# Optimization experiments

Hardware: AMD Instinct MI355X
Metric: run time of the kernel (lower is better)

## Reference

```python
import jax, jax.numpy as jnp
import numpy as np
from jax import lax

B, IN_CH, OUT_CH, H, W = 32, 128, 256, 64, 64
STYLE_CH, TDIM, G = 512, 512, 32
GN_EPS, MOD_EPS = 1e-5, 1e-8
DN = ('NCHW', 'OIHW', 'NCHW')


def swish(x):
    return x * jax.nn.sigmoid(x)


def group_norm(x, gamma, beta):
    n, c, h, w = x.shape
    xr = x.reshape(n, G, c // G, h, w)
    mu = xr.mean(axis=(2, 3, 4), keepdims=True)
    var = xr.var(axis=(2, 3, 4), keepdims=True)
    xn = ((xr - mu) * lax.rsqrt(var + GN_EPS)).reshape(n, c, h, w)
    return xn * gamma[None, :, None, None] + beta[None, :, None, None]


def conv3x3(x, w, b):
    y = lax.conv_general_dilated(x, w, (1, 1), ((1, 1), (1, 1)), dimension_numbers=DN)
    return y + b[None, :, None, None]


def setup_inputs() -> dict:
    key = jax.random.key(0)
    ks = jax.random.split(key, 16)
    s = 0.05
    return {
        'x': jax.random.normal(ks[0], (B, IN_CH, H, W), jnp.float32),
        'temb': jax.random.normal(ks[1], (B, TDIM), jnp.float32),
        'style': jax.random.normal(ks[2], (B, STYLE_CH), jnp.float32),
        'gn1_g': jnp.ones((IN_CH,), jnp.float32),
        'gn1_b': jnp.zeros((IN_CH,), jnp.float32),
        'conv1_w': jax.random.normal(ks[3], (OUT_CH, IN_CH, 3, 3), jnp.float32) * s,
        'conv1_b': jnp.zeros((OUT_CH,), jnp.float32),
        'temb_w': jax.random.normal(ks[4], (OUT_CH, TDIM), jnp.float32) * s,
        'temb_b': jnp.zeros((OUT_CH,), jnp.float32),
        'gn2_g': jnp.ones((OUT_CH,), jnp.float32),
        'gn2_b': jnp.zeros((OUT_CH,), jnp.float32),
        'style_w': jax.random.normal(ks[5], (OUT_CH, STYLE_CH), jnp.float32) * s,
        'style_b': jnp.zeros((OUT_CH,), jnp.float32),
        'mod_w': jax.random.normal(ks[6], (OUT_CH, OUT_CH, 3, 3), jnp.float32) * s,
        'sc_w': jax.random.normal(ks[7], (OUT_CH, IN_CH, 1, 1), jnp.float32) * s,
        'sc_b': jnp.zeros((OUT_CH,), jnp.float32),
    }


def reference(x, temb, style, gn1_g, gn1_b, conv1_w, conv1_b, temb_w, temb_b,
              gn2_g, gn2_b, style_w, style_b, mod_w, sc_w, sc_b):
    # block1: GN -> Swish -> Conv3x3
    h = conv3x3(swish(group_norm(x, gn1_g, gn1_b)), conv1_w, conv1_b)
    # temb projection: Swish -> Linear, broadcast over HxW
    h = h + (swish(temb) @ temb_w.T + temb_b)[:, :, None, None]
    # block2: GN -> Swish -> Dropout(0) [identity]
    h = swish(group_norm(h, gn2_g, gn2_b))
    # modulated + demodulated per-sample conv (StyleGAN2-style)
    style2 = style @ style_w.T + style_b                       # (b, out_ch)
    wmod = mod_w[None] * (style2[:, None, :, None, None] + 1.0)  # (b, o, i, kh, kw)
    d = lax.rsqrt((wmod ** 2).sum(axis=(2, 3, 4), keepdims=True) + MOD_EPS)
    wmod = wmod * d
    conv1s = lambda xi, wi: lax.conv_general_dilated(
        xi[None], wi, (1, 1), ((1, 1), (1, 1)), dimension_numbers=DN)[0]
    h = jax.vmap(conv1s)(h, wmod)                              # per-sample conv
    # shortcut 1x1 conv (in_ch != out_ch)
    sc = lax.conv_general_dilated(x, sc_w, (1, 1), ((0, 0), (0, 0)), dimension_numbers=DN)
    sc = sc + sc_b[None, :, None, None]
    return h + sc
```

## Files before the change

### kernel.cpp

```cpp
#include <hip/hip_runtime.h>
#include <cstdint>

typedef unsigned short u16;
typedef unsigned int   u32;

typedef __attribute__((ext_vector_type(8))) short bf16x8;
typedef __attribute__((ext_vector_type(4))) float f32x4;

#define DEV __device__ __forceinline__

static constexpr int HP = 66, WP = 66;

DEV u16 f2bf(float f) {
  u32 u = __float_as_uint(f);
  u32 r = (u + 0x7fffu + ((u >> 16) & 1u)) >> 16;
  return (u16)r;
}
DEV float bf2f(u16 v) { return __uint_as_float((u32)v << 16); }

DEV void gload_lds16(const void* g, void* s) {
  __builtin_amdgcn_global_load_lds(
      (const __attribute__((address_space(1))) void*)g,
      (__attribute__((address_space(3))) void*)s, 16, 0, 0);
}

__global__ __launch_bounds__(256) void repack_w_kernel(const float* __restrict__ src,
                                                       u16* __restrict__ dst,
                                                       int Cin, int K, int total,
                                                       int ksq, int kdim) {
  for (int idx = blockIdx.x * 256 + threadIdx.x; idx < total; idx += gridDim.x * 256) {
    int co = idx / K;
    int r  = idx - co * K;
    int s  = r / Cin;
    int ci = r - s * Cin;
    int ky = s / kdim, kx = s - ky * kdim;
    dst[idx] = f2bf(src[(co * Cin + ci) * ksq + ky * kdim + kx]);
  }
}

__global__ __launch_bounds__(256) void modw_ss_kernel(const float* __restrict__ w,
                                                      float* __restrict__ SS_T) {
  int o = blockIdx.x, i = threadIdx.x;
  const float* p = w + (size_t)(o * 256 + i) * 9;
  float s = 0.f;
#pragma unroll
  for (int k = 0; k < 9; ++k) s += p[k] * p[k];
  SS_T[i * 256 + o] = s;
}

__global__ __launch_bounds__(256) void style_mvec_kernel(const float* __restrict__ style,
                                                         const float* __restrict__ style_w,
                                                         const float* __restrict__ style_b,
                                                         float* __restrict__ mvec) {
  __shared__ float st[512];
  int b = blockIdx.x, t = threadIdx.x;
  for (int k = t; k < 512; k += 256) st[k] = style[b * 512 + k];
  __syncthreads();
  const float4* wr = (const float4*)(style_w + t * 512);
  float acc = 0.f;
  for (int k = 0; k < 128; ++k) {
    float4 w4 = wr[k];
    acc += w4.x * st[k*4] + w4.y * st[k*4+1] + w4.z * st[k*4+2] + w4.w * st[k*4+3];
  }
  mvec[b * 256 + t] = acc + style_b[t] + 1.f;
}

__global__ __launch_bounds__(256) void demod_kernel(const float* __restrict__ mvec,
                                                    const float* __restrict__ SS_T,
                                                    float* __restrict__ dvec) {
  __shared__ float m2[256];
  int b = blockIdx.x, t = threadIdx.x;
  float mv = mvec[b * 256 + t];
  m2[t] = mv * mv;
  __syncthreads();
  float acc = 0.f;
  for (int i = 0; i < 256; ++i) acc += m2[i] * SS_T[i * 256 + t];
  dvec[b * 256 + t] = rsqrtf(acc + 1e-8f);
}

__global__ __launch_bounds__(256) void scale_sc_kernel(const float* __restrict__ sc_w,
                                                       const float* __restrict__ dvec,
                                                       u16* __restrict__ scTb) {
  int idx = blockIdx.x * 256 + threadIdx.x;
  int ci = idx & 127;
  int co = (idx >> 7) & 255;
  int b  = idx >> 15;
  scTb[idx] = f2bf(sc_w[co * 128 + ci] / dvec[b * 256 + co]);
}

__global__ __launch_bounds__(256) void temb_proj_kernel(const float* __restrict__ temb,
                                                        const float* __restrict__ temb_w,
                                                        const float* __restrict__ temb_b,
                                                        const float* __restrict__ conv1_b,
                                                        float* __restrict__ tb2) {
  __shared__ float sw[512];
  int b = blockIdx.x, t = threadIdx.x;
  for (int k = t; k < 512; k += 256) {
    float v = temb[b * 512 + k];
    sw[k] = v / (1.f + __expf(-v));
  }
  __syncthreads();
  const float4* wr = (const float4*)(temb_w + t * 512);
  float acc = 0.f;
  for (int k = 0; k < 128; ++k) {
    float4 w4 = wr[k];
    acc += w4.x * sw[k*4] + w4.y * sw[k*4+1] + w4.z * sw[k*4+2] + w4.w * sw[k*4+3];
  }
  tb2[b * 256 + t] = acc + temb_b[t] + conv1_b[t];
}

template <int C>
__global__ __launch_bounds__(256) void halo_zero_kernel(u16* __restrict__ buf) {
  int idx = blockIdx.x * 256 + threadIdx.x;
  const int GR = C / 8;
  if (idx >= 32 * 260 * GR) return;
  int g = idx % GR;
  int p = (idx / GR) % 260;
  int b = idx / (GR * 260);
  int y, x;
  if (p < 66)       { y = 0;        x = p; }
  else if (p < 132) { y = 65;       x = p - 66; }
  else if (p < 196) { y = p - 131;  x = 0; }
  else              { y = p - 195;  x = 65; }
  uint4 z; z.x = 0; z.y = 0; z.z = 0; z.w = 0;
  *(uint4*)(buf + (((size_t)b * HP + y) * WP + x) * C + g * 8) = z;
}

__global__ __launch_bounds__(256) void gn1_stats_kernel(const float* __restrict__ x,
                                                        float2* __restrict__ st1) {
  int bg = blockIdx.x;
  const float4* p = (const float4*)(x + (size_t)bg * 16384);
  float s = 0.f, s2 = 0.f;
  for (int i = threadIdx.x; i < 4096; i += 256) {
    float4 v = p[i];
    s  += v.x + v.y + v.z + v.w;
    s2 += v.x*v.x + v.y*v.y + v.z*v.z + v.w*v.w;
  }
  for (int d = 32; d; d >>= 1) { s += __shfl_down(s, d); s2 += __shfl_down(s2, d); }
  __shared__ float red[2][4];
  if ((threadIdx.x & 63) == 0) { red[0][threadIdx.x >> 6] = s; red[1][threadIdx.x >> 6] = s2; }
  __syncthreads();
  if (threadIdx.x == 0) {
    s  = red[0][0] + red[0][1] + red[0][2] + red[0][3];
    s2 = red[1][0] + red[1][1] + red[1][2] + red[1][3];
    float mean = s / 16384.f;
    float var  = s2 / 16384.f - mean * mean;
    st1[bg] = make_float2(mean, rsqrtf(var + 1e-5f));
  }
}

__global__ __launch_bounds__(256) void gn1_apply_kernel(const float* __restrict__ x,
                                                        const float2* __restrict__ st1,
                                                        const float* __restrict__ g1,
                                                        const float* __restrict__ b1,
                                                        u16* __restrict__ act1p,
                                                        u16* __restrict__ xh) {
  __shared__ float xs[128][65];
  int blk = blockIdx.x;
  int b = blk >> 6, y = blk & 63;
  int t = threadIdx.x;
#pragma unroll 8
  for (int pass = 0; pass < 32; ++pass) {
    int c = pass * 4 + (t >> 6);
    xs[c][t & 63] = x[(((size_t)b * 128 + c) * 64 + y) * 64 + (t & 63)];
  }
  __syncthreads();
  for (int pass = 0; pass < 32; ++pass) {
    int xc = pass * 2 + (t >> 7);
    int c  = t & 127;
    float v = xs[c][xc];
    float2 ms = st1[b * 32 + (c >> 2)];
    float vn = (v - ms.x) * ms.y * g1[c] + b1[c];
    float sw = vn / (1.f + __expf(-vn));
    act1p[(((size_t)b * HP + (y + 1)) * WP + (xc + 1)) * 128 + c] = f2bf(sw);
    xh[(((size_t)b * 64 + y) * 64 + xc) * 128 + c] = f2bf(v);
  }
}

__global__ void gn2_final_kernel(const float* __restrict__ st2sum, float2* __restrict__ st2) {
  int idx = blockIdx.x * 256 + threadIdx.x;
  if (idx >= 1024) return;
  float s  = st2sum[idx * 2];
  float s2 = st2sum[idx * 2 + 1];
  float mean = s / 32768.f;
  float var  = s2 / 32768.f - mean * mean;
  st2[idx] = make_float2(mean, rsqrtf(var + 1e-5f));
}

__global__ __launch_bounds__(256) void gn2_apply_kernel(const u16* __restrict__ h1,
                                                        const float2* __restrict__ st2,
                                                        const float* __restrict__ g2,
                                                        const float* __restrict__ b2,
                                                        const float* __restrict__ mvec,
                                                        u16* __restrict__ act2p) {
  int idx = blockIdx.x * 256 + threadIdx.x;
  int gpix = idx >> 5;
  int gi = idx & 31;
  int c0 = gi * 8;
  int b = gpix >> 12, y = (gpix >> 6) & 63, x = gpix & 63;
  uint4 raw = *(const uint4*)(h1 + (size_t)gpix * 256 + c0);
  const u16* rs = (const u16*)&raw;
  float2 ms = st2[b * 32 + gi];
  const float* mv = mvec + b * 256 + c0;
  u16 outp[8];
#pragma unroll
  for (int e = 0; e < 8; ++e) {
    float v  = bf2f(rs[e]);
    float vn = (v - ms.x) * ms.y * g2[c0 + e] + b2[c0 + e];
    float sw = vn / (1.f + __expf(-vn));
    outp[e] = f2bf(sw * mv[e]);
  }
  *(uint4*)(act2p + (((size_t)b * HP + (y + 1)) * WP + (x + 1)) * 256 + c0) = *(const uint4*)outp;
}

template <int MODE>
__global__ __launch_bounds__(512, 2) void igemm_kernel(const u16* __restrict__ act,
                                                       const u16* __restrict__ wT,
                                                       const float* __restrict__ epi,
                                                       const u16* __restrict__ xh,
                                                       const u16* __restrict__ scTb,
                                                       const float* __restrict__ sc_b,
                                                       u16* __restrict__ h1out,
                                                       float* __restrict__ fout,
                                                       float* __restrict__ st2sum) {
  constexpr int CIN    = (MODE == 0) ? 128 : 256;
  constexpr int NSUB   = CIN / 64;
  constexpr int KW     = CIN * 9;
  constexpr int NKMAIN = KW / 64;
  constexpr int NKT    = (MODE == 2) ? NKMAIN + 2 : NKMAIN;

  __shared__ __align__(16) unsigned char lds[131072];
  const int tid  = threadIdx.x;
  const int wave = tid >> 6, lane = tid & 63;
  const int wm = wave >> 2, wn = wave & 3;
  const int m_base = blockIdx.x * 256;
  const int bimg = m_base >> 12;
  const int ln = lane & 15, l4 = lane >> 4;

  const int srow = lane >> 3;
  const int glog = (lane & 7) ^ srow;

  u32 pixA[2][2], pixX[2][2], rowB[2][2], rowS[2][2];
#pragma unroll
  for (int j = 0; j < 2; ++j)
#pragma unroll
    for (int h = 0; h < 2; ++h) {
      int mlocal = (wave & 3) * 16 + j * 8 + srow + h * 64 + (wave >> 2) * 128;
      int m = m_base + mlocal;
      int y = (m >> 6) & 63, x = m & 63;
      pixA[j][h] = (u32)((bimg * HP + y) * WP + x) * CIN + glog * 8;
      if (MODE == 2) pixX[j][h] = (u32)m * 128 + glog * 8;
      int co = (wave >> 1) * 64 + h * 32 + (wave & 1) * 16 + j * 8 + srow;
      rowB[j][h] = (u32)co * KW + glog * 8;
      if (MODE == 2) rowS[j][h] = (u32)(bimg * 256 + co) * 128 + glog * 8;
    }

  f32x4 acc[8][4];
#pragma unroll
  for (int i = 0; i < 8; ++i)
#pragma unroll
    for (int j = 0; j < 4; ++j) acc[i][j] = (f32x4){0.f, 0.f, 0.f, 0.f};

  auto stageA = [&](int kt, int h, int buf) {
    unsigned char* dst = lds + buf * 65536 + h * 16384 + wave * 2048;
    if (MODE == 2 && kt >= NKMAIN) {
      u32 ko = (u32)(kt - NKMAIN) * 64;
      gload_lds16(xh + pixX[0][h] + ko, dst);
      gload_lds16(xh + pixX[1][h] + ko, dst + 1024);
    } else {
      int tap = kt / NSUB;
      int kin = (kt - tap * NSUB) * 64;
      int ky = tap / 3, kx = tap - ky * 3;
      u32 ko = (u32)((ky * WP + kx) * CIN + kin);
      gload_lds16(act + pixA[0][h] + ko, dst);
      gload_lds16(act + pixA[1][h] + ko, dst + 1024);
    }
  };
  auto stageB = [&](int kt, int g, int buf) {
    unsigned char* dst = lds + buf * 65536 + 32768 + g * 16384 + wave * 2048;
    if (MODE == 2 && kt >= NKMAIN) {
      u32 ko = (u32)(kt - NKMAIN) * 64;
      gload_lds16(scTb + rowS[0][g] + ko, dst);
      gload_lds16(scTb + rowS[1][g] + ko, dst + 1024);
    } else {
      u32 ko = (u32)kt * 64;
      gload_lds16(wT + rowB[0][g] + ko, dst);
      gload_lds16(wT + rowB[1][g] + ko, dst + 1024);
    }
  };

  bf16x8 af[8], bf[4];
  auto ldA = [&](int h, int buf) {
    const unsigned char* As = lds + buf * 65536;
#pragma unroll
    for (int f = 0; f < 4; ++f)
#pragma unroll
      for (int kk = 0; kk < 2; ++kk) {
        int lr = h * 128 + wm * 64 + f * 16 + ln;
        int gr = (kk * 4 + l4) ^ (ln & 7);
        af[f * 2 + kk] = *(const bf16x8*)(As + lr * 128 + gr * 16);
      }
  };
  auto ldB = [&](int g, int buf) {
    const unsigned char* Bs = lds + buf * 65536 + 32768;
#pragma unroll
    for (int f1 = 0; f1 < 2; ++f1)
#pragma unroll
      for (int kk = 0; kk < 2; ++kk) {
        int lr = g * 128 + wn * 32 + f1 * 16 + ln;
        int gr = (kk * 4 + l4) ^ (ln & 7);
        bf[f1 * 2 + kk] = *(const bf16x8*)(Bs + lr * 128 + gr * 16);
      }
  };
  auto mmac = [&](int h, int g) {
    __builtin_amdgcn_s_setprio(1);
#pragma unroll
    for (int f = 0; f < 4; ++f)
#pragma unroll
      for (int f1 = 0; f1 < 2; ++f1)
#pragma unroll
        for (int kk = 0; kk < 2; ++kk)
          acc[h * 4 + f][g * 2 + f1] = __builtin_amdgcn_mfma_f32_16x16x32_bf16(
              af[f * 2 + kk], bf[f1 * 2 + kk], acc[h * 4 + f][g * 2 + f1], 0, 0, 0);
    __builtin_amdgcn_s_setprio(0);
  };

#define PHASE_BAR() do { __builtin_amdgcn_sched_barrier(0); \
    __builtin_amdgcn_s_barrier(); __builtin_amdgcn_sched_barrier(0); } while (0)

  stageA(0, 0, 0); stageB(0, 0, 0); stageB(0, 1, 0); stageA(0, 1, 0);

#pragma unroll 2
  for (int kt = 0; kt < NKT - 1; ++kt) {
    const int cur = kt & 1, nxt = cur ^ 1;
    stageA(kt + 1, 0, nxt);
    asm volatile("s_waitcnt vmcnt(6)" ::: "memory");
    PHASE_BAR();
    ldB(0, cur); ldA(0, cur);
    mmac(0, 0);
    stageB(kt + 1, 0, nxt);
    asm volatile("s_waitcnt vmcnt(6)" ::: "memory");
    PHASE_BAR();
    ldB(1, cur);
    mmac(0, 1);
    stageB(kt + 1, 1, nxt);
    asm volatile("s_waitcnt vmcnt(6)" ::: "memory");
    PHASE_BAR();
    ldA(1, cur);
    mmac(1, 1);
    stageA(kt + 1, 1, nxt);
    PHASE_BAR();
    ldB(0, cur);
    mmac(1, 0);
  }
  {
    const int cur = (NKT - 1) & 1;
    asm volatile("s_waitcnt vmcnt(4)" ::: "memory");
    PHASE_BAR();
    ldB(0, cur); ldA(0, cur); mmac(0, 0);
    asm volatile("s_waitcnt vmcnt(2)" ::: "memory");
    PHASE_BAR();
    ldB(1, cur); mmac(0, 1);
    asm volatile("s_waitcnt vmcnt(0)" ::: "memory");
    PHASE_BAR();
    ldA(1, cur); mmac(1, 1);
    PHASE_BAR();
    ldB(0, cur); mmac(1, 0);
  }
#undef PHASE_BAR

  if (MODE == 0) {
    const float* tbrow = epi + bimg * 256;
    float ps[4], ps2[4];
#pragma unroll
    for (int fn = 0; fn < 4; ++fn) { ps[fn] = 0.f; ps2[fn] = 0.f; }
#pragma unroll
    for (int fm = 0; fm < 8; ++fm)
#pragma unroll
      for (int fn = 0; fn < 4; ++fn) {
        int co = wn * 64 + fn * 16 + ln;
        float add = tbrow[co];
#pragma unroll
        for (int i = 0; i < 4; ++i) {
          int m = m_base + wm * 128 + fm * 16 + (l4 << 2) + i;
          float v = acc[fm][fn][i] + add;
          h1out[(size_t)m * 256 + co] = f2bf(v);
          ps[fn] += v; ps2[fn] += v * v;
        }
      }
#pragma unroll
    for (int fn = 0; fn < 4; ++fn) {
      float s = ps[fn], s2 = ps2[fn];
      s += __shfl_xor(s, 1);  s2 += __shfl_xor(s2, 1);
      s += __shfl_xor(s, 2);  s2 += __shfl_xor(s2, 2);
      s += __shfl_xor(s, 4);  s2 += __shfl_xor(s2, 4);
      s += __shfl_xor(s, 16); s2 += __shfl_xor(s2, 16);
      s += __shfl_xor(s, 32); s2 += __shfl_xor(s2, 32);
      if ((lane & 55) == 0) {
        int g = wn * 8 + fn * 2 + (ln >> 3);
        atomicAdd(&st2sum[bimg * 64 + g * 2 + 0], s);
        atomicAdd(&st2sum[bimg * 64 + g * 2 + 1], s2);
      }
    }
  } else {
    float* tile = (float*)lds;
    const int pixb = m_base & 4095;
#pragma unroll
    for (int c = 0; c < 4; ++c) {
      __syncthreads();
      if (wn == c) {
#pragma unroll
        for (int fn = 0; fn < 4; ++fn) {
          int nl = fn * 16 + ln;
          int co = c * 64 + nl;
          float dsc = epi[bimg * 256 + co];
          float scb = sc_b[co];
#pragma unroll
          for (int fm = 0; fm < 8; ++fm)
#pragma unroll
            for (int i = 0; i < 4; ++i) {
              int ml = wm * 128 + fm * 16 + (l4 << 2) + i;
              tile[nl * 257 + ml] = acc[fm][fn][i] * dsc + scb;
            }
        }
      }
      __syncthreads();
#pragma unroll 4
      for (int it = 0; it < 32; ++it) {
        int lin = it * 512 + tid;
        int co_l = lin >> 8, ml = lin & 255;
        fout[((size_t)(bimg * 256 + c * 64 + co_l)) * 4096 + pixb + ml] =
            tile[co_l * 257 + ml];
      }
    }
  }
}

extern "C" void kernel_launch(void* const* d_in, const int* in_sizes, int n_in,
                              void* d_out, int out_size, void* d_ws, size_t ws_size,
                              hipStream_t stream) {
  const float* x       = (const float*)d_in[0];
  const float* temb    = (const float*)d_in[1];
  const float* style   = (const float*)d_in[2];
  const float* gn1_g   = (const float*)d_in[3];
  const float* gn1_b   = (const float*)d_in[4];
  const float* conv1_w = (const float*)d_in[5];
  const float* conv1_b = (const float*)d_in[6];
  const float* temb_w  = (const float*)d_in[7];
  const float* temb_b  = (const float*)d_in[8];
  const float* gn2_g   = (const float*)d_in[9];
  const float* gn2_b   = (const float*)d_in[10];
  const float* style_w = (const float*)d_in[11];
  const float* style_b = (const float*)d_in[12];
  const float* mod_w   = (const float*)d_in[13];
  const float* sc_w    = (const float*)d_in[14];
  const float* sc_b    = (const float*)d_in[15];
  float* out = (float*)d_out;
  char* ws = (char*)d_ws;

  size_t o = 0;
  auto alloc = [&](size_t bytes) { size_t r = o; o += (bytes + 255) & ~(size_t)255; return r; };
  const size_t act1p_bytes = (size_t)32 * HP * WP * 128 * 2;
  const size_t xh_bytes    = (size_t)32 * 64 * 64 * 128 * 2;
  const size_t h1_bytes    = (size_t)32 * 4096 * 256 * 2;
  const size_t act2p_bytes = (size_t)32 * HP * WP * 256 * 2;
  size_t o_act1p = alloc(act1p_bytes);
  size_t o_xh    = alloc(xh_bytes);
  size_t o_h1    = alloc(h1_bytes);
  size_t o_act2p = alloc(act2p_bytes);
  size_t o_w1T   = alloc((size_t)256 * 1152 * 2);
  size_t o_wmT   = alloc((size_t)256 * 2304 * 2);
  size_t o_scTb  = alloc((size_t)32 * 256 * 128 * 2);
  size_t o_tb2   = alloc(8192 * 4);
  size_t o_mvec  = alloc(8192 * 4);
  size_t o_dvec  = alloc(8192 * 4);
  size_t o_SS    = alloc((size_t)256 * 256 * 4);
  size_t o_st1   = alloc(1024 * 8);
  size_t o_st2   = alloc(1024 * 8);
  size_t o_s2sum = alloc(32 * 32 * 2 * 4);
  if (ws_size < o) return;

  u16*    act1p = (u16*)(ws + o_act1p);
  u16*    xh    = (u16*)(ws + o_xh);
  u16*    h1    = (u16*)(ws + o_h1);
  u16*    act2p = (u16*)(ws + o_act2p);
  u16*    w1T   = (u16*)(ws + o_w1T);
  u16*    wmT   = (u16*)(ws + o_wmT);
  u16*    scTb  = (u16*)(ws + o_scTb);
  float*  tb2   = (float*)(ws + o_tb2);
  float*  mvec  = (float*)(ws + o_mvec);
  float*  dvec  = (float*)(ws + o_dvec);
  float*  SS_T  = (float*)(ws + o_SS);
  float2* st1   = (float2*)(ws + o_st1);
  float2* st2   = (float2*)(ws + o_st2);
  float*  s2sum = (float*)(ws + o_s2sum);

  halo_zero_kernel<128><<<(32 * 260 * 16 + 255) / 256, 256, 0, stream>>>(act1p);
  halo_zero_kernel<256><<<(32 * 260 * 32 + 255) / 256, 256, 0, stream>>>(act2p);
  hipMemsetAsync(s2sum, 0, 32 * 32 * 2 * 4, stream);

  repack_w_kernel<<<1152, 256, 0, stream>>>(conv1_w, w1T, 128, 1152, 256 * 1152, 9, 3);
  repack_w_kernel<<<2304, 256, 0, stream>>>(mod_w, wmT, 256, 2304, 256 * 2304, 9, 3);
  modw_ss_kernel<<<256, 256, 0, stream>>>(mod_w, SS_T);
  temb_proj_kernel<<<32, 256, 0, stream>>>(temb, temb_w, temb_b, conv1_b, tb2);
  style_mvec_kernel<<<32, 256, 0, stream>>>(style, style_w, style_b, mvec);
  demod_kernel<<<32, 256, 0, stream>>>(mvec, SS_T, dvec);
  scale_sc_kernel<<<4096, 256, 0, stream>>>(sc_w, dvec, scTb);
  gn1_stats_kernel<<<1024, 256, 0, stream>>>(x, st1);
  gn1_apply_kernel<<<2048, 256, 0, stream>>>(x, st1, gn1_g, gn1_b, act1p, xh);

  igemm_kernel<0><<<512, 512, 0, stream>>>(act1p, w1T, tb2, nullptr, nullptr,
                                           nullptr, h1, nullptr, s2sum);

  gn2_final_kernel<<<4, 256, 0, stream>>>(s2sum, st2);
  gn2_apply_kernel<<<16384, 256, 0, stream>>>(h1, st2, gn2_g, gn2_b, mvec, act2p);

  igemm_kernel<2><<<512, 512, 0, stream>>>(act2p, wmT, dvec, xh, scTb,
                                           sc_b, nullptr, out, nullptr);
}
```

Baseline: 375.0 us.

## Deepen implicit-GEMM prefetch into a 10-slot LDS ring and fold GN2 finalize

The conv implicit-GEMM main loop moves from two 64KB LDS buffers to a ring of ten 16KB slots, 160KB in total. A and B half-tiles for the next one to two k-steps are now issued earlier and waited on with relaxed vmcnt thresholds, so global-to-LDS loads can overlap more MFMA work. The swizzle index now uses the local row, and a separate tail handles the last two iterations. The small gn2_final kernel is removed: gn2_apply computes mean and rstd directly from the raw sums, saving one launch and one buffer at the cost of redundant per-thread math. The larger LDS footprint leaves no slack for a second block per CU, and the hand-tuned wait counts are fragile.

```diff
diff --git a/kernel.cpp b/kernel.cpp
--- a/kernel.cpp
+++ b/kernel.cpp
@@ -177,18 +177,8 @@
   }
 }
 
-__global__ void gn2_final_kernel(const float* __restrict__ st2sum, float2* __restrict__ st2) {
-  int idx = blockIdx.x * 256 + threadIdx.x;
-  if (idx >= 1024) return;
-  float s  = st2sum[idx * 2];
-  float s2 = st2sum[idx * 2 + 1];
-  float mean = s / 32768.f;
-  float var  = s2 / 32768.f - mean * mean;
-  st2[idx] = make_float2(mean, rsqrtf(var + 1e-5f));
-}
-
 __global__ __launch_bounds__(256) void gn2_apply_kernel(const u16* __restrict__ h1,
-                                                        const float2* __restrict__ st2,
+                                                        const float* __restrict__ st2sum,
                                                         const float* __restrict__ g2,
                                                         const float* __restrict__ b2,
                                                         const float* __restrict__ mvec,
@@ -200,13 +190,16 @@
   int b = gpix >> 12, y = (gpix >> 6) & 63, x = gpix & 63;
   uint4 raw = *(const uint4*)(h1 + (size_t)gpix * 256 + c0);
   const u16* rs = (const u16*)&raw;
-  float2 ms = st2[b * 32 + gi];
+  float s  = st2sum[b * 64 + gi * 2];
+  float s2 = st2sum[b * 64 + gi * 2 + 1];
+  float mean = s / 32768.f;
+  float rstd = rsqrtf(s2 / 32768.f - mean * mean + 1e-5f);
   const float* mv = mvec + b * 256 + c0;
   u16 outp[8];
 #pragma unroll
   for (int e = 0; e < 8; ++e) {
     float v  = bf2f(rs[e]);
-    float vn = (v - ms.x) * ms.y * g2[c0 + e] + b2[c0 + e];
+    float vn = (v - mean) * rstd * g2[c0 + e] + b2[c0 + e];
     float sw = vn / (1.f + __expf(-vn));
     outp[e] = f2bf(sw * mv[e]);
   }
@@ -229,7 +222,7 @@
   constexpr int NKMAIN = KW / 64;
   constexpr int NKT    = (MODE == 2) ? NKMAIN + 2 : NKMAIN;
 
-  __shared__ __align__(16) unsigned char lds[131072];
+  __shared__ __align__(16) unsigned char lds[163840];
   const int tid  = threadIdx.x;
   const int wave = tid >> 6, lane = tid & 63;
   const int wm = wave >> 2, wn = wave & 3;
@@ -261,8 +254,8 @@
 #pragma unroll
     for (int j = 0; j < 4; ++j) acc[i][j] = (f32x4){0.f, 0.f, 0.f, 0.f};
 
-  auto stageA = [&](int kt, int h, int buf) {
-    unsigned char* dst = lds + buf * 65536 + h * 16384 + wave * 2048;
+  auto stageA = [&](int kt, int h, int slotbyte) {
+    unsigned char* dst = lds + slotbyte + wave * 2048;
     if (MODE == 2 && kt >= NKMAIN) {
       u32 ko = (u32)(kt - NKMAIN) * 64;
       gload_lds16(xh + pixX[0][h] + ko, dst);
@@ -276,8 +269,8 @@
       gload_lds16(act + pixA[1][h] + ko, dst + 1024);
     }
   };
-  auto stageB = [&](int kt, int g, int buf) {
-    unsigned char* dst = lds + buf * 65536 + 32768 + g * 16384 + wave * 2048;
+  auto stageB = [&](int kt, int g, int slotbyte) {
+    unsigned char* dst = lds + slotbyte + wave * 2048;
     if (MODE == 2 && kt >= NKMAIN) {
       u32 ko = (u32)(kt - NKMAIN) * 64;
       gload_lds16(scTb + rowS[0][g] + ko, dst);
@@ -290,25 +283,25 @@
   };
 
   bf16x8 af[8], bf[4];
-  auto ldA = [&](int h, int buf) {
-    const unsigned char* As = lds + buf * 65536;
+  auto ldA = [&](int slotbyte) {
+    const unsigned char* As = lds + slotbyte;
 #pragma unroll
     for (int f = 0; f < 4; ++f)
 #pragma unroll
       for (int kk = 0; kk < 2; ++kk) {
-        int lr = h * 128 + wm * 64 + f * 16 + ln;
-        int gr = (kk * 4 + l4) ^ (ln & 7);
+        int lr = wm * 64 + f * 16 + ln;
+        int gr = (kk * 4 + l4) ^ (lr & 7);
         af[f * 2 + kk] = *(const bf16x8*)(As + lr * 128 + gr * 16);
       }
   };
-  auto ldB = [&](int g, int buf) {
-    const unsigned char* Bs = lds + buf * 65536 + 32768;
+  auto ldB = [&](int slotbyte) {
+    const unsigned char* Bs = lds + slotbyte;
 #pragma unroll
     for (int f1 = 0; f1 < 2; ++f1)
 #pragma unroll
       for (int kk = 0; kk < 2; ++kk) {
-        int lr = g * 128 + wn * 32 + f1 * 16 + ln;
-        int gr = (kk * 4 + l4) ^ (ln & 7);
+        int lr = wn * 32 + f1 * 16 + ln;
+        int gr = (kk * 4 + l4) ^ (lr & 7);
         bf[f1 * 2 + kk] = *(const bf16x8*)(Bs + lr * 128 + gr * 16);
       }
   };
@@ -327,47 +320,65 @@
 
 #define PHASE_BAR() do { __builtin_amdgcn_sched_barrier(0); \
     __builtin_amdgcn_s_barrier(); __builtin_amdgcn_sched_barrier(0); } while (0)
-
-  stageA(0, 0, 0); stageB(0, 0, 0); stageB(0, 1, 0); stageA(0, 1, 0);
-
+#define VMC(n) asm volatile("s_waitcnt vmcnt(" #n ")" ::: "memory")
+
+  stageA(0, 0, 0 * 16384); stageB(0, 0, 1 * 16384);
+  stageB(0, 1, 2 * 16384); stageA(0, 1, 3 * 16384);
+  stageA(1, 0, 4 * 16384); stageB(1, 0, 5 * 16384); stageB(1, 1, 6 * 16384);
+
+  auto md = [](int x) { return x >= 10 ? x - 10 : x; };
+
+  int sb = 0;
 #pragma unroll 2
-  for (int kt = 0; kt < NKT - 1; ++kt) {
-    const int cur = kt & 1, nxt = cur ^ 1;
-    stageA(kt + 1, 0, nxt);
-    asm volatile("s_waitcnt vmcnt(6)" ::: "memory");
+  for (int kt = 0; kt < NKT - 2; ++kt) {
+    const int sA0 = sb * 16384, sB0 = md(sb + 1) * 16384;
+    const int sB1 = md(sb + 2) * 16384, sA1 = md(sb + 3) * 16384;
+    VMC(10); PHASE_BAR();
+    stageA(kt + 1, 1, md(sb + 7) * 16384);
+    ldB(sB0); ldA(sA0);
+    mmac(0, 0);
+    VMC(10); PHASE_BAR();
+    stageA(kt + 2, 0, md(sb + 8) * 16384);
+    ldB(sB1);
+    mmac(0, 1);
+    VMC(10); PHASE_BAR();
+    stageB(kt + 2, 0, md(sb + 9) * 16384);
+    ldA(sA1);
+    mmac(1, 1);
     PHASE_BAR();
-    ldB(0, cur); ldA(0, cur);
-    mmac(0, 0);
-    stageB(kt + 1, 0, nxt);
-    asm volatile("s_waitcnt vmcnt(6)" ::: "memory");
+    stageB(kt + 2, 1, md(sb + 10) * 16384);
+    ldB(sB0);
+    mmac(1, 0);
+    sb = md(sb + 4);
+  }
+  {
+    const int sA0 = sb * 16384, sB0 = md(sb + 1) * 16384;
+    const int sB1 = md(sb + 2) * 16384, sA1 = md(sb + 3) * 16384;
+    VMC(10); PHASE_BAR();
+    stageA(NKT - 1, 1, md(sb + 7) * 16384);
+    ldB(sB0); ldA(sA0); mmac(0, 0);
+    VMC(10); PHASE_BAR();
+    ldB(sB1); mmac(0, 1);
+    VMC(8); PHASE_BAR();
+    ldA(sA1); mmac(1, 1);
     PHASE_BAR();
-    ldB(1, cur);
-    mmac(0, 1);
-    stageB(kt + 1, 1, nxt);
-    asm volatile("s_waitcnt vmcnt(6)" ::: "memory");
+    ldB(sB0); mmac(1, 0);
+    sb = md(sb + 4);
+  }
+  {
+    const int sA0 = sb * 16384, sB0 = md(sb + 1) * 16384;
+    const int sB1 = md(sb + 2) * 16384, sA1 = md(sb + 3) * 16384;
+    VMC(4); PHASE_BAR();
+    ldB(sB0); ldA(sA0); mmac(0, 0);
+    VMC(2); PHASE_BAR();
+    ldB(sB1); mmac(0, 1);
+    VMC(0); PHASE_BAR();
+    ldA(sA1); mmac(1, 1);
     PHASE_BAR();
-    ldA(1, cur);
-    mmac(1, 1);
-    stageA(kt + 1, 1, nxt);
-    PHASE_BAR();
-    ldB(0, cur);
-    mmac(1, 0);
-  }
-  {
-    const int cur = (NKT - 1) & 1;
-    asm volatile("s_waitcnt vmcnt(4)" ::: "memory");
-    PHASE_BAR();
-    ldB(0, cur); ldA(0, cur); mmac(0, 0);
-    asm volatile("s_waitcnt vmcnt(2)" ::: "memory");
-    PHASE_BAR();
-    ldB(1, cur); mmac(0, 1);
-    asm volatile("s_waitcnt vmcnt(0)" ::: "memory");
-    PHASE_BAR();
-    ldA(1, cur); mmac(1, 1);
-    PHASE_BAR();
-    ldB(0, cur); mmac(1, 0);
+    ldB(sB0); mmac(1, 0);
   }
 #undef PHASE_BAR
+#undef VMC
 
   if (MODE == 0) {
     const float* tbrow = epi + bimg * 256;
@@ -476,7 +487,6 @@
   size_t o_dvec  = alloc(8192 * 4);
   size_t o_SS    = alloc((size_t)256 * 256 * 4);
   size_t o_st1   = alloc(1024 * 8);
-  size_t o_st2   = alloc(1024 * 8);
   size_t o_s2sum = alloc(32 * 32 * 2 * 4);
   if (ws_size < o) return;
 
@@ -492,7 +502,6 @@
   float*  dvec  = (float*)(ws + o_dvec);
   float*  SS_T  = (float*)(ws + o_SS);
   float2* st1   = (float2*)(ws + o_st1);
-  float2* st2   = (float2*)(ws + o_st2);
   float*  s2sum = (float*)(ws + o_s2sum);
 
   halo_zero_kernel<128><<<(32 * 260 * 16 + 255) / 256, 256, 0, stream>>>(act1p);
@@ -512,8 +521,7 @@
   igemm_kernel<0><<<512, 512, 0, stream>>>(act1p, w1T, tb2, nullptr, nullptr,
                                            nullptr, h1, nullptr, s2sum);
 
-  gn2_final_kernel<<<4, 256, 0, stream>>>(s2sum, st2);
-  gn2_apply_kernel<<<16384, 256, 0, stream>>>(h1, st2, gn2_g, gn2_b, mvec, act2p);
+  gn2_apply_kernel<<<16384, 256, 0, stream>>>(h1, s2sum, gn2_g, gn2_b, mvec, act2p);
 
   igemm_kernel<2><<<512, 512, 0, stream>>>(act2p, wmT, dvec, xh, scTb,
                                            sc_b, nullptr, out, nullptr);
```

New measurement: 514.7 us. 1.37x slower.

## Switch implicit-GEMM to 32x32x16 MFMA and fold GN2 finalize into apply

Applied to the files above, without the earlier changes.

Replaces the 16x16x32 bf16 MFMA tiling in both convolution GEMMs with 32x32x16 MFMAs. The LDS fragment loads, accumulator layout, epilogue indexing and GroupNorm statistic shuffle reduction are rewritten to match. This cuts LDS fragment reads per MFMA, and B fragments are held in two register sets so the final B reload per k-step is dropped. Separately, the tiny gn2_final kernel is removed and mean/rstd are computed inline in gn2_apply, saving one launch at the cost of redundant per-thread math.

```diff
diff --git a/kernel.cpp b/kernel.cpp
--- a/kernel.cpp
+++ b/kernel.cpp
@@ -4,8 +4,9 @@
 typedef unsigned short u16;
 typedef unsigned int   u32;
 
-typedef __attribute__((ext_vector_type(8))) short bf16x8;
-typedef __attribute__((ext_vector_type(4))) float f32x4;
+typedef __attribute__((ext_vector_type(8)))  short bf16x8;
+typedef __attribute__((ext_vector_type(4)))  float f32x4;
+typedef __attribute__((ext_vector_type(16))) float f32x16;
 
 #define DEV __device__ __forceinline__
 
@@ -177,18 +178,8 @@
   }
 }
 
-__global__ void gn2_final_kernel(const float* __restrict__ st2sum, float2* __restrict__ st2) {
-  int idx = blockIdx.x * 256 + threadIdx.x;
-  if (idx >= 1024) return;
-  float s  = st2sum[idx * 2];
-  float s2 = st2sum[idx * 2 + 1];
-  float mean = s / 32768.f;
-  float var  = s2 / 32768.f - mean * mean;
-  st2[idx] = make_float2(mean, rsqrtf(var + 1e-5f));
-}
-
 __global__ __launch_bounds__(256) void gn2_apply_kernel(const u16* __restrict__ h1,
-                                                        const float2* __restrict__ st2,
+                                                        const float* __restrict__ st2sum,
                                                         const float* __restrict__ g2,
                                                         const float* __restrict__ b2,
                                                         const float* __restrict__ mvec,
@@ -200,13 +191,16 @@
   int b = gpix >> 12, y = (gpix >> 6) & 63, x = gpix & 63;
   uint4 raw = *(const uint4*)(h1 + (size_t)gpix * 256 + c0);
   const u16* rs = (const u16*)&raw;
-  float2 ms = st2[b * 32 + gi];
+  float s  = st2sum[b * 64 + gi * 2];
+  float s2 = st2sum[b * 64 + gi * 2 + 1];
+  float mean = s / 32768.f;
+  float rstd = rsqrtf(s2 / 32768.f - mean * mean + 1e-5f);
   const float* mv = mvec + b * 256 + c0;
   u16 outp[8];
 #pragma unroll
   for (int e = 0; e < 8; ++e) {
     float v  = bf2f(rs[e]);
-    float vn = (v - ms.x) * ms.y * g2[c0 + e] + b2[c0 + e];
+    float vn = (v - mean) * rstd * g2[c0 + e] + b2[c0 + e];
     float sw = vn / (1.f + __expf(-vn));
     outp[e] = f2bf(sw * mv[e]);
   }
@@ -235,7 +229,7 @@
   const int wm = wave >> 2, wn = wave & 3;
   const int m_base = blockIdx.x * 256;
   const int bimg = m_base >> 12;
-  const int ln = lane & 15, l4 = lane >> 4;
+  const int l31 = lane & 31, l5 = lane >> 5;
 
   const int srow = lane >> 3;
   const int glog = (lane & 7) ^ srow;
@@ -255,11 +249,13 @@
       if (MODE == 2) rowS[j][h] = (u32)(bimg * 256 + co) * 128 + glog * 8;
     }
 
-  f32x4 acc[8][4];
-#pragma unroll
-  for (int i = 0; i < 8; ++i)
-#pragma unroll
-    for (int j = 0; j < 4; ++j) acc[i][j] = (f32x4){0.f, 0.f, 0.f, 0.f};
+  f32x16 acc32[4][2];
+#pragma unroll
+  for (int i = 0; i < 4; ++i)
+#pragma unroll
+    for (int j = 0; j < 2; ++j)
+#pragma unroll
+      for (int e = 0; e < 16; ++e) acc32[i][j][e] = 0.f;
 
   auto stageA = [&](int kt, int h, int buf) {
     unsigned char* dst = lds + buf * 65536 + h * 16384 + wave * 2048;
@@ -289,39 +285,35 @@
     }
   };
 
-  bf16x8 af[8], bf[4];
-  auto ldA = [&](int h, int buf) {
-    const unsigned char* As = lds + buf * 65536;
-#pragma unroll
-    for (int f = 0; f < 4; ++f)
-#pragma unroll
-      for (int kk = 0; kk < 2; ++kk) {
-        int lr = h * 128 + wm * 64 + f * 16 + ln;
-        int gr = (kk * 4 + l4) ^ (ln & 7);
-        af[f * 2 + kk] = *(const bf16x8*)(As + lr * 128 + gr * 16);
+  bf16x8 af[8], bf0[4], bf1[4];
+  auto ldA32 = [&](int h, int buf) {
+    const unsigned char* As = lds + buf * 65536 + h * 16384;
+#pragma unroll
+    for (int rb2 = 0; rb2 < 2; ++rb2)
+#pragma unroll
+      for (int ks = 0; ks < 4; ++ks) {
+        int row = wm * 64 + rb2 * 32 + l31;
+        int gr  = (ks * 2 + l5) ^ (lane & 7);
+        af[rb2 * 4 + ks] = *(const bf16x8*)(As + row * 128 + gr * 16);
       }
   };
-  auto ldB = [&](int g, int buf) {
-    const unsigned char* Bs = lds + buf * 65536 + 32768;
-#pragma unroll
-    for (int f1 = 0; f1 < 2; ++f1)
-#pragma unroll
-      for (int kk = 0; kk < 2; ++kk) {
-        int lr = g * 128 + wn * 32 + f1 * 16 + ln;
-        int gr = (kk * 4 + l4) ^ (ln & 7);
-        bf[f1 * 2 + kk] = *(const bf16x8*)(Bs + lr * 128 + gr * 16);
-      }
+  auto ldB32 = [&](int g, int buf, bf16x8* bfr) {
+    const unsigned char* Bs = lds + buf * 65536 + 32768 + g * 16384;
+    int row = wn * 32 + l31;
+#pragma unroll
+    for (int ks = 0; ks < 4; ++ks) {
+      int gr = (ks * 2 + l5) ^ (lane & 7);
+      bfr[ks] = *(const bf16x8*)(Bs + row * 128 + gr * 16);
+    }
   };
-  auto mmac = [&](int h, int g) {
+  auto mmac32 = [&](int h, int g, bf16x8* bfr) {
     __builtin_amdgcn_s_setprio(1);
 #pragma unroll
-    for (int f = 0; f < 4; ++f)
-#pragma unroll
-      for (int f1 = 0; f1 < 2; ++f1)
-#pragma unroll
-        for (int kk = 0; kk < 2; ++kk)
-          acc[h * 4 + f][g * 2 + f1] = __builtin_amdgcn_mfma_f32_16x16x32_bf16(
-              af[f * 2 + kk], bf[f1 * 2 + kk], acc[h * 4 + f][g * 2 + f1], 0, 0, 0);
+    for (int rb2 = 0; rb2 < 2; ++rb2)
+#pragma unroll
+      for (int ks = 0; ks < 4; ++ks)
+        acc32[h * 2 + rb2][g] = __builtin_amdgcn_mfma_f32_32x32x16_bf16(
+            af[rb2 * 4 + ks], bfr[ks], acc32[h * 2 + rb2][g], 0, 0, 0);
     __builtin_amdgcn_s_setprio(0);
   };
 
@@ -336,68 +328,67 @@
     stageA(kt + 1, 0, nxt);
     asm volatile("s_waitcnt vmcnt(6)" ::: "memory");
     PHASE_BAR();
-    ldB(0, cur); ldA(0, cur);
-    mmac(0, 0);
+    ldB32(0, cur, bf0); ldA32(0, cur);
+    mmac32(0, 0, bf0);
     stageB(kt + 1, 0, nxt);
     asm volatile("s_waitcnt vmcnt(6)" ::: "memory");
     PHASE_BAR();
-    ldB(1, cur);
-    mmac(0, 1);
+    ldB32(1, cur, bf1);
+    mmac32(0, 1, bf1);
     stageB(kt + 1, 1, nxt);
     asm volatile("s_waitcnt vmcnt(6)" ::: "memory");
     PHASE_BAR();
-    ldA(1, cur);
-    mmac(1, 1);
+    ldA32(1, cur);
+    mmac32(1, 1, bf1);
     stageA(kt + 1, 1, nxt);
     PHASE_BAR();
-    ldB(0, cur);
-    mmac(1, 0);
+    mmac32(1, 0, bf0);
   }
   {
     const int cur = (NKT - 1) & 1;
     asm volatile("s_waitcnt vmcnt(4)" ::: "memory");
     PHASE_BAR();
-    ldB(0, cur); ldA(0, cur); mmac(0, 0);
+    ldB32(0, cur, bf0); ldA32(0, cur); mmac32(0, 0, bf0);
     asm volatile("s_waitcnt vmcnt(2)" ::: "memory");
     PHASE_BAR();
-    ldB(1, cur); mmac(0, 1);
+    ldB32(1, cur, bf1); mmac32(0, 1, bf1);
     asm volatile("s_waitcnt vmcnt(0)" ::: "memory");
     PHASE_BAR();
-    ldA(1, cur); mmac(1, 1);
-    PHASE_BAR();
-    ldB(0, cur); mmac(1, 0);
+    ldA32(1, cur); mmac32(1, 1, bf1);
+    PHASE_BAR();
+    mmac32(1, 0, bf0);
   }
 #undef PHASE_BAR
 
   if (MODE == 0) {
     const float* tbrow = epi + bimg * 256;
-    float ps[4], ps2[4];
-#pragma unroll
-    for (int fn = 0; fn < 4; ++fn) { ps[fn] = 0.f; ps2[fn] = 0.f; }
-#pragma unroll
-    for (int fm = 0; fm < 8; ++fm)
-#pragma unroll
-      for (int fn = 0; fn < 4; ++fn) {
-        int co = wn * 64 + fn * 16 + ln;
+    float ps[2], ps2[2];
+#pragma unroll
+    for (int cb = 0; cb < 2; ++cb) { ps[cb] = 0.f; ps2[cb] = 0.f; }
+#pragma unroll
+    for (int rb = 0; rb < 4; ++rb)
+#pragma unroll
+      for (int cb = 0; cb < 2; ++cb) {
+        int co = wn * 64 + cb * 32 + l31;
         float add = tbrow[co];
 #pragma unroll
-        for (int i = 0; i < 4; ++i) {
-          int m = m_base + wm * 128 + fm * 16 + (l4 << 2) + i;
-          float v = acc[fm][fn][i] + add;
+        for (int i = 0; i < 16; ++i) {
+          int row = (i & 3) + 8 * (i >> 2) + 4 * l5;
+          int m = m_base + wm * 128 + rb * 32 + row;
+          float v = acc32[rb][cb][i] + add;
           h1out[(size_t)m * 256 + co] = f2bf(v);
-          ps[fn] += v; ps2[fn] += v * v;
+          ps[cb] += v; ps2[cb] += v * v;
         }
       }
 #pragma unroll
-    for (int fn = 0; fn < 4; ++fn) {
-      float s = ps[fn], s2 = ps2[fn];
+    for (int cb = 0; cb < 2; ++cb) {
+      float s = ps[cb], s2 = ps2[cb];
       s += __shfl_xor(s, 1);  s2 += __shfl_xor(s2, 1);
       s += __shfl_xor(s, 2);  s2 += __shfl_xor(s2, 2);
       s += __shfl_xor(s, 4);  s2 += __shfl_xor(s2, 4);
-      s += __shfl_xor(s, 16); s2 += __shfl_xor(s2, 16);
       s += __shfl_xor(s, 32); s2 += __shfl_xor(s2, 32);
-      if ((lane & 55) == 0) {
-        int g = wn * 8 + fn * 2 + (ln >> 3);
+      if ((lane & 39) == 0) {
+        int g = wn * 8 + cb * 4 + (l31 >> 3);
         atomicAdd(&st2sum[bimg * 64 + g * 2 + 0], s);
         atomicAdd(&st2sum[bimg * 64 + g * 2 + 1], s2);
       }
@@ -410,17 +401,17 @@
       __syncthreads();
       if (wn == c) {
 #pragma unroll
-        for (int fn = 0; fn < 4; ++fn) {
-          int nl = fn * 16 + ln;
+        for (int cb = 0; cb < 2; ++cb) {
+          int nl = cb * 32 + l31;
           int co = c * 64 + nl;
           float dsc = epi[bimg * 256 + co];
           float scb = sc_b[co];
 #pragma unroll
-          for (int fm = 0; fm < 8; ++fm)
-#pragma unroll
-            for (int i = 0; i < 4; ++i) {
-              int ml = wm * 128 + fm * 16 + (l4 << 2) + i;
-              tile[nl * 257 + ml] = acc[fm][fn][i] * dsc + scb;
+          for (int rb = 0; rb < 4; ++rb)
+#pragma unroll
+            for (int i = 0; i < 16; ++i) {
+              int ml = wm * 128 + rb * 32 + (i & 3) + 8 * (i >> 2) + 4 * l5;
+              tile[nl * 257 + ml] = acc32[rb][cb][i] * dsc + scb;
             }
         }
       }
@@ -476,7 +467,6 @@
   size_t o_dvec  = alloc(8192 * 4);
   size_t o_SS    = alloc((size_t)256 * 256 * 4);
   size_t o_st1   = alloc(1024 * 8);
-  size_t o_st2   = alloc(1024 * 8);
   size_t o_s2sum = alloc(32 * 32 * 2 * 4);
   if (ws_size < o) return;
 
@@ -492,7 +482,6 @@
   float*  dvec  = (float*)(ws + o_dvec);
   float*  SS_T  = (float*)(ws + o_SS);
   float2* st1   = (float2*)(ws + o_st1);
-  float2* st2   = (float2*)(ws + o_st2);
   float*  s2sum = (float*)(ws + o_s2sum);
 
   halo_zero_kernel<128><<<(32 * 260 * 16 + 255) / 256, 256, 0, stream>>>(act1p);
@@ -512,8 +501,7 @@
   igemm_kernel<0><<<512, 512, 0, stream>>>(act1p, w1T, tb2, nullptr, nullptr,
                                            nullptr, h1, nullptr, s2sum);
 
-  gn2_final_kernel<<<4, 256, 0, stream>>>(s2sum, st2);
-  gn2_apply_kernel<<<16384, 256, 0, stream>>>(h1, st2, gn2_g, gn2_b, mvec, act2p);
+  gn2_apply_kernel<<<16384, 256, 0, stream>>>(h1, s2sum, gn2_g, gn2_b, mvec, act2p);
 
   igemm_kernel<2><<<512, 512, 0, stream>>>(act2p, wmT, dvec, xh, scTb,
                                            sc_b, nullptr, out, nullptr);
```

Result: slower. 405.7 us (+8.2%).
